# Kernel tuning notes

Hardware: AMD Instinct MI355X
Metric: run time of the kernel (lower is better)

Reference implementation:

```python
import jax, jax.numpy as jnp
import numpy as np

B, S, D, H = 2, 2048, 1024, 16
DH = D // H  # 64


def setup_inputs() -> dict:
    key = jax.random.key(0)
    ks = jax.random.split(key, 12)
    inp = {
        "hidden_states": jax.random.normal(ks[0], (B, S, D), dtype=jnp.float32),
        "attention_mask": jax.random.randint(ks[1], (B, S), 0, 2, dtype=jnp.int32),
        "Wq": jax.random.normal(ks[2], (D, D), dtype=jnp.float32) / np.sqrt(D),
        "bq": jnp.zeros((D,), dtype=jnp.float32),
        "Wk": jax.random.normal(ks[3], (D, D), dtype=jnp.float32) / np.sqrt(D),
        "bk": jnp.zeros((D,), dtype=jnp.float32),
        "Wv": jax.random.normal(ks[4], (D, D), dtype=jnp.float32) / np.sqrt(D),
        "bv": jnp.zeros((D,), dtype=jnp.float32),
        # per-head additive query bias (emotion manipulation path)
        "emotion_w": jax.random.normal(ks[5], (H, DH), dtype=jnp.float32),
        "Wo": jax.random.normal(ks[6], (D, D), dtype=jnp.float32) / np.sqrt(D),
        "bo": jnp.zeros((D,), dtype=jnp.float32),
    }
    return inp


def reference(hidden_states, attention_mask, Wq, bq, Wk, bk, Wv, bv, emotion_w, Wo, bo):
    b, s, d = hidden_states.shape
    # projections -> [b, h, s, dh]
    def proj(W, bias):
        y = hidden_states @ W + bias
        return y.reshape(b, s, H, DH).transpose(0, 2, 1, 3)

    q = proj(Wq, bq)
    k = proj(Wk, bk)
    v = proj(Wv, bv)

    # manipulation_type='emotion': additive per-head query bias
    q = q + emotion_w[None, :, None, :]

    scores = jnp.einsum("bhqd,bhkd->bhqk", q, k) / np.sqrt(DH).astype(np.float32)
    # key-padding mask: positions where mask==0 get -inf
    scores = jnp.where(attention_mask[:, None, None, :] == 0, -jnp.inf, scores)
    attn = jax.nn.softmax(scores, axis=-1)  # dropout is identity in eval mode

    out = jnp.einsum("bhqk,bhkd->bhqd", attn, v)
    out = out.transpose(0, 2, 1, 3).reshape(b, s, d)
    return out @ Wo + bo
```

## Files before the change

### kernel.cpp

```cpp
#include <hip/hip_runtime.h>
#include <hip/hip_bf16.h>


#define B_  2
#define S_  2048
#define D_  1024
#define K_  1024
#define H_  16
#define DH_ 64
#define BS_ (B_*S_)

typedef __hip_bfloat16 bf16;
typedef __attribute__((ext_vector_type(8))) short s8v;
typedef __attribute__((ext_vector_type(4))) short s4v;
typedef __attribute__((ext_vector_type(4))) float f4v;

__device__ __forceinline__ float b2f(bf16 x) { return __bfloat162float(x); }
__device__ __forceinline__ bf16  f2b(float x) { return __float2bfloat16(x); }

__device__ __forceinline__ void gl_lds_16B(const bf16* g, bf16* l) {
    __builtin_amdgcn_global_load_lds(
        (const __attribute__((address_space(1))) unsigned int*)g,
        (__attribute__((address_space(3))) unsigned int*)l, 16, 0, 0);
}

#define QSCALE_ 0.1803368801f

__global__ __launch_bounds__(256) void prep_kernel(
    const float* __restrict__ X, const int* __restrict__ mask,
    const float* __restrict__ Wq, const float* __restrict__ Wk,
    const float* __restrict__ Wv, const float* __restrict__ Wo,
    bf16* __restrict__ Xb, bf16* __restrict__ mkbf,
    bf16* __restrict__ WTq, bf16* __restrict__ WTk,
    bf16* __restrict__ WTv, bf16* __restrict__ WTo)
{
    __shared__ float Ls[64][68];
    const int blk = blockIdx.x;
    const int t   = threadIdx.x;

    if (blk < 1024) {
        const int z   = blk >> 8;
        const int t16 = blk & 255;
        const int k0  = (t16 >> 4) * 64;
        const int n0  = (t16 & 15) * 64;
        const float* __restrict__ W = (z == 0) ? Wq : (z == 1) ? Wk : (z == 2) ? Wv : Wo;
        bf16* __restrict__ WT       = (z == 0) ? WTq : (z == 1) ? WTk : (z == 2) ? WTv : WTo;

        const int lr = t >> 4;
        const int lc = (t & 15) * 4;
        #pragma unroll
        for (int i = 0; i < 4; i++) {
            const int k = i * 16 + lr;
            const float4 v = *(const float4*)(W + (size_t)(k0 + k) * K_ + n0 + lc);
            Ls[k][lc + 0] = v.x; Ls[k][lc + 1] = v.y;
            Ls[k][lc + 2] = v.z; Ls[k][lc + 3] = v.w;
        }
        __syncthreads();
        #pragma unroll
        for (int i = 0; i < 4; i++) {
            const int n = i * 16 + lr;
            s4v o;
            #pragma unroll
            for (int j = 0; j < 4; j++) {
                bf16 tb = f2b(Ls[lc + j][n]);
                o[j] = *(short*)&tb;
            }
            *(s4v*)(WT + (size_t)(n0 + n) * K_ + k0 + lc) = o;
        }
    } else if (blk < 5120) {
        const size_t idx = ((size_t)(blk - 1024) * 256 + t) * 4;
        const float4 v = *(const float4*)(X + idx);
        bf16 t0 = f2b(v.x), t1 = f2b(v.y), t2 = f2b(v.z), t3 = f2b(v.w);
        s4v o;
        o[0] = *(short*)&t0; o[1] = *(short*)&t1;
        o[2] = *(short*)&t2; o[3] = *(short*)&t3;
        *(s4v*)(Xb + idx) = o;
    } else {
        const int idx = (blk - 5120) * 256 + t;
        mkbf[idx] = f2b(mask[idx] ? 1.0f : 0.0f);
    }
}

template <bool SWAPPED>
__device__ __forceinline__ void gemm_tile(
    const bf16* __restrict__ A, const bf16* __restrict__ BT,
    int m0, int n0, bf16* As, bf16* Bs, f4v acc[4][4])
{
    const int t    = threadIdx.x;
    const int lane = t & 63;
    const int wave = t >> 6;
    const int quad = lane >> 4;
    const int l15  = lane & 15;
    const int wr   = wave >> 1;
    const int wc   = wave & 1;

    const int sr = t >> 3;
    const int sc = (t & 7) * 8;

    for (int kb = 0; kb < K_; kb += 64) {
        #pragma unroll
        for (int i = 0; i < 4; i++) {
            const int r = i * 32 + sr;
            gl_lds_16B(A  + (size_t)(m0 + r) * K_ + kb + sc, As + r * 64 + sc);
            gl_lds_16B(BT + (size_t)(n0 + r) * K_ + kb + sc, Bs + r * 64 + sc);
        }
        __syncthreads();

        #pragma unroll
        for (int ks = 0; ks < 2; ks++) {
            s8v fA[4], fB[4];
            #pragma unroll
            for (int i = 0; i < 4; i++) {
                fA[i] = *(const s8v*)&As[(wr * 64 + i * 16 + l15) * 64 + ks * 32 + quad * 8];
                fB[i] = *(const s8v*)&Bs[(wc * 64 + i * 16 + l15) * 64 + ks * 32 + quad * 8];
            }
            #pragma unroll
            for (int i = 0; i < 4; i++)
                #pragma unroll
                for (int j = 0; j < 4; j++)
                    acc[i][j] = SWAPPED
                        ? __builtin_amdgcn_mfma_f32_16x16x32_bf16(fB[i], fA[j], acc[i][j], 0, 0, 0)
                        : __builtin_amdgcn_mfma_f32_16x16x32_bf16(fA[i], fB[j], acc[i][j], 0, 0, 0);
        }
        __syncthreads();
    }
}

__global__ __launch_bounds__(256) void proj_qkv_kernel(
    const bf16* __restrict__ Xb,
    const bf16* __restrict__ WTq, const float* __restrict__ bq,
    const bf16* __restrict__ WTk, const float* __restrict__ bk,
    const bf16* __restrict__ WTv, const float* __restrict__ bv,
    const float* __restrict__ emo, const int* __restrict__ mask,
    bf16* __restrict__ q_ws, bf16* __restrict__ k_ws, bf16* __restrict__ v_ws)
{
    const int m0 = blockIdx.x * 128;
    const int n0 = blockIdx.y * 128;
    const int z  = blockIdx.z;

    __shared__ __align__(16) bf16 As[128 * 64];
    __shared__ __align__(16) bf16 Bs[128 * 64];

    const int t    = threadIdx.x;
    const int lane = t & 63;
    const int wave = t >> 6;
    const int quad = lane >> 4;
    const int l15  = lane & 15;
    const int wr   = wave >> 1;
    const int wc   = wave & 1;

    f4v acc[4][4] = {};

    if (z == 0) {
        gemm_tile<false>(Xb, WTq, m0, n0, As, Bs, acc);
        #pragma unroll
        for (int j = 0; j < 4; j++) {
            const int n  = n0 + wc * 64 + j * 16 + l15;
            const int h  = n >> 6, dh = n & 63;
            const float bias_n = bq[n] + emo[n];
            #pragma unroll
            for (int i = 0; i < 4; i++) {
                #pragma unroll
                for (int r = 0; r < 4; r++) {
                    const int m = m0 + wr * 64 + i * 16 + quad * 4 + r;
                    const int b = m >> 11, s = m & 2047;
                    q_ws[(((size_t)(b * H_ + h)) * S_ + s) * DH_ + dh] =
                        f2b((acc[i][j][r] + bias_n) * QSCALE_);
                }
            }
        }
    } else if (z == 1) {
        gemm_tile<false>(Xb, WTk, m0, n0, As, Bs, acc);
        #pragma unroll
        for (int j = 0; j < 4; j++) {
            const int n  = n0 + wc * 64 + j * 16 + l15;
            const int h  = n >> 6, dh = n & 63;
            const float bias_n = bk[n];
            #pragma unroll
            for (int i = 0; i < 4; i++) {
                #pragma unroll
                for (int r = 0; r < 4; r++) {
                    const int m = m0 + wr * 64 + i * 16 + quad * 4 + r;
                    const int b = m >> 11, s = m & 2047;
                    k_ws[(((size_t)(b * H_ + h)) * S_ + s) * DH_ + dh] =
                        f2b(acc[i][j][r] + bias_n);
                }
            }
        }
    } else {
        gemm_tile<true>(Xb, WTv, m0, n0, As, Bs, acc);
        #pragma unroll
        for (int j = 0; j < 4; j++) {
            const int m = m0 + wr * 64 + j * 16 + l15;
            const int b = m >> 11, s = m & 2047;
            const float msk = mask[b * S_ + s] ? 1.0f : 0.0f;
            #pragma unroll
            for (int i = 0; i < 4; i++) {
                #pragma unroll
                for (int r = 0; r < 4; r++) {
                    const int n  = n0 + wc * 64 + i * 16 + quad * 4 + r;
                    const int h  = n >> 6, dh = n & 63;
                    v_ws[(((size_t)(b * H_ + h)) * DH_ + dh) * S_ + s] =
                        f2b((acc[i][j][r] + bv[n]) * msk);
                }
            }
        }
    }
}

__global__ __launch_bounds__(256) void proj_out_kernel(
    const bf16* __restrict__ ctx, const bf16* __restrict__ WTo,
    const float* __restrict__ bo, float* __restrict__ out)
{
    const int m0 = blockIdx.x * 128;
    const int n0 = blockIdx.y * 128;

    __shared__ __align__(16) bf16 As[128 * 64];
    __shared__ __align__(16) bf16 Bs[128 * 64];

    const int t    = threadIdx.x;
    const int lane = t & 63;
    const int wave = t >> 6;
    const int quad = lane >> 4;
    const int l15  = lane & 15;
    const int wr   = wave >> 1;
    const int wc   = wave & 1;

    f4v acc[4][4] = {};
    gemm_tile<false>(ctx, WTo, m0, n0, As, Bs, acc);

    #pragma unroll
    for (int j = 0; j < 4; j++) {
        const int n = n0 + wc * 64 + j * 16 + l15;
        const float bias_n = bo[n];
        #pragma unroll
        for (int i = 0; i < 4; i++) {
            #pragma unroll
            for (int r = 0; r < 4; r++) {
                const int m = m0 + wr * 64 + i * 16 + quad * 4 + r;
                out[(size_t)m * D_ + n] = acc[i][j][r] + bias_n;
            }
        }
    }
}

#define PP_ 88

__global__ __launch_bounds__(512) void attn_kernel(
    const bf16* __restrict__ q_ws, const bf16* __restrict__ k_ws,
    const bf16* __restrict__ v_ws, const bf16* __restrict__ mkbf,
    bf16* __restrict__ ctx)
{
    const int bh = blockIdx.x;
    const int q0 = blockIdx.y * 128;
    const int b  = bh >> 4;
    const int h  = bh & 15;

    __shared__ __align__(16) bf16 k_lds[2][64 * 64];
    __shared__ __align__(16) bf16 vt_lds[2][64 * 64];
    __shared__ __align__(16) bf16 p_lds[8][16 * PP_];

    const int t    = threadIdx.x;
    const int wave = t >> 6;
    const int lane = t & 63;
    const int quad = lane >> 4;
    const int l15  = lane & 15;
    const int lxor = l15 & 7;

    s8v qf[2];
    #pragma unroll
    for (int dt = 0; dt < 2; dt++)
        qf[dt] = *(const s8v*)(q_ws +
            ((size_t)bh * S_ + q0 + wave * 16 + l15) * DH_ + dt * 32 + quad * 8);

    f4v oacc[4] = {};
    f4v osum   = {};

    const int r_st  = t >> 3;
    const int cs_st = (t & 7) ^ (r_st & 7);
    const int e_st  = t * 8;

    auto stage = [&](int kb0, bf16* kd, bf16* vd) {
        gl_lds_16B(k_ws + ((size_t)bh * S_ + kb0 + r_st) * DH_ + cs_st * 8,
                   kd + e_st);
        gl_lds_16B(v_ws + ((size_t)bh * DH_ + r_st) * S_ + kb0 + cs_st * 8,
                   vd + e_st);
    };

    stage(0, k_lds[0], vt_lds[0]);
    __syncthreads();

    int cur = 0;
    for (int kb0 = 0; kb0 < S_; kb0 += 64) {
        if (kb0 + 64 < S_)
            stage(kb0 + 64, k_lds[cur ^ 1], vt_lds[cur ^ 1]);

        const bf16* __restrict__ kc = k_lds[cur];
        const bf16* __restrict__ vc = vt_lds[cur];

        f4v sacc[4] = {};
        __builtin_amdgcn_s_setprio(1);
        #pragma unroll
        for (int kt = 0; kt < 4; kt++) {
            #pragma unroll
            for (int dt = 0; dt < 2; dt++) {
                const s8v kf = *(const s8v*)&kc[(kt * 16 + l15) * 64 +
                                                ((dt * 4 + quad) ^ lxor) * 8];
                sacc[kt] = __builtin_amdgcn_mfma_f32_16x16x32_bf16(kf, qf[dt], sacc[kt], 0, 0, 0);
            }
        }
        __builtin_amdgcn_s_setprio(0);

        #pragma unroll
        for (int kt = 0; kt < 4; kt++) {
            float2 e01, e23;
            e01.x = exp2f(sacc[kt][0]);
            e01.y = exp2f(sacc[kt][1]);
            e23.x = exp2f(sacc[kt][2]);
            e23.y = exp2f(sacc[kt][3]);
            union { __hip_bfloat162 hh; unsigned u; } lo, hi;
            lo.hh = __float22bfloat162_rn(e01);
            hi.hh = __float22bfloat162_rn(e23);
            *(uint2*)&p_lds[wave][l15 * PP_ + kt * 16 + quad * 4] =
                make_uint2(lo.u, hi.u);
        }

        __builtin_amdgcn_s_waitcnt(0xC07F);

        #pragma unroll
        for (int kh = 0; kh < 2; kh++) {
            const s8v ap = *(const s8v*)&p_lds[wave][l15 * PP_ + kh * 32 + quad * 8];
            const s8v mv = *(const s8v*)(mkbf + (size_t)b * S_ + kb0 + kh * 32 + quad * 8);
            __builtin_amdgcn_s_setprio(1);
            #pragma unroll
            for (int nt = 0; nt < 4; nt++) {
                const s8v vf = *(const s8v*)&vc[(nt * 16 + l15) * 64 +
                                                ((kh * 4 + quad) ^ lxor) * 8];
                oacc[nt] = __builtin_amdgcn_mfma_f32_16x16x32_bf16(ap, vf, oacc[nt], 0, 0, 0);
            }
            osum = __builtin_amdgcn_mfma_f32_16x16x32_bf16(ap, mv, osum, 0, 0, 0);
            __builtin_amdgcn_s_setprio(0);
        }

        __syncthreads();
        cur ^= 1;
    }

    #pragma unroll
    for (int r = 0; r < 4; r++) {
        const float inv = 1.0f / osum[r];
        const int q = q0 + wave * 16 + quad * 4 + r;
        #pragma unroll
        for (int nt = 0; nt < 4; nt++)
            ctx[((size_t)b * S_ + q) * D_ + h * DH_ + nt * 16 + l15] =
                f2b(oacc[nt][r] * inv);
    }
}

extern "C" void kernel_launch(void* const* d_in, const int* in_sizes, int n_in,
                              void* d_out, int out_size, void* d_ws, size_t ws_size,
                              hipStream_t stream) {
    (void)in_sizes; (void)n_in; (void)out_size; (void)ws_size;

    const float* X    = (const float*)d_in[0];
    const int*   mask = (const int*)d_in[1];
    const float* Wq   = (const float*)d_in[2];
    const float* bq   = (const float*)d_in[3];
    const float* Wk   = (const float*)d_in[4];
    const float* bk   = (const float*)d_in[5];
    const float* Wv   = (const float*)d_in[6];
    const float* bv   = (const float*)d_in[7];
    const float* emo  = (const float*)d_in[8];
    const float* Wo   = (const float*)d_in[9];
    const float* bo   = (const float*)d_in[10];
    float* out = (float*)d_out;

    bf16* q_ws = (bf16*)d_ws;
    bf16* k_ws = q_ws + (size_t)BS_ * D_;
    bf16* v_ws = k_ws + (size_t)BS_ * D_;
    bf16* ctx  = v_ws + (size_t)BS_ * D_;
    bf16* Xb   = ctx  + (size_t)BS_ * D_;
    bf16* WTq  = Xb   + (size_t)BS_ * D_;
    bf16* WTk  = WTq  + (size_t)D_ * K_;
    bf16* WTv  = WTk  + (size_t)D_ * K_;
    bf16* WTo  = WTv  + (size_t)D_ * K_;
    bf16* mkbf = WTo  + (size_t)D_ * K_;

    hipLaunchKernelGGL(prep_kernel, dim3(5136), dim3(256), 0, stream,
                       X, mask, Wq, Wk, Wv, Wo, Xb, mkbf, WTq, WTk, WTv, WTo);
    hipLaunchKernelGGL(proj_qkv_kernel, dim3(BS_ / 128, D_ / 128, 3), dim3(256), 0, stream,
                       Xb, WTq, bq, WTk, bk, WTv, bv, emo, mask, q_ws, k_ws, v_ws);
    hipLaunchKernelGGL(attn_kernel, dim3(B_ * H_, S_ / 128), dim3(512), 0, stream,
                       q_ws, k_ws, v_ws, mkbf, ctx);
    hipLaunchKernelGGL(proj_out_kernel, dim3(BS_ / 128, D_ / 128), dim3(256), 0, stream,
                       ctx, WTo, bo, out);
}
```

Before: 226.5 us.

## Rewrite attention with 32x32 MFMA tiles and direct global K/V fragment loads

The attention kernel moves from 16x16x32 MFMA tiles and 8 waves of 16 queries to 32x32x16 MFMA tiles and 4 waves of 32 queries each. K and V fragments are read straight from global memory (cache) instead of being staged into double-buffered LDS, which removes the per-block __syncthreads. The P tile is double-buffered by loop parity with an XOR swizzle. This trades away LDS staging and block-wide K/V sharing for fewer barriers and larger MFMA tiles, at the cost of more global/L2 traffic and fewer waves per block.

```diff
diff --git a/kernel.cpp b/kernel.cpp
--- a/kernel.cpp
+++ b/kernel.cpp
@@ -14,6 +14,7 @@
 typedef __attribute__((ext_vector_type(8))) short s8v;
 typedef __attribute__((ext_vector_type(4))) short s4v;
 typedef __attribute__((ext_vector_type(4))) float f4v;
+typedef __attribute__((ext_vector_type(16))) float f16v;
 
 __device__ __forceinline__ float b2f(bf16 x) { return __bfloat162float(x); }
 __device__ __forceinline__ bf16  f2b(float x) { return __float2bfloat16(x); }
@@ -244,9 +245,9 @@
     }
 }
 
-#define PP_ 88
-
-__global__ __launch_bounds__(512) void attn_kernel(
+#define PQ_ 2048
+
+__global__ __launch_bounds__(256) void attn_kernel(
     const bf16* __restrict__ q_ws, const bf16* __restrict__ k_ws,
     const bf16* __restrict__ v_ws, const bf16* __restrict__ mkbf,
     bf16* __restrict__ ctx)
@@ -256,104 +257,86 @@
     const int b  = bh >> 4;
     const int h  = bh & 15;
 
-    __shared__ __align__(16) bf16 k_lds[2][64 * 64];
-    __shared__ __align__(16) bf16 vt_lds[2][64 * 64];
-    __shared__ __align__(16) bf16 p_lds[8][16 * PP_];
+    __shared__ __align__(16) bf16 p_lds[2 * 4 * PQ_];
 
     const int t    = threadIdx.x;
     const int wave = t >> 6;
     const int lane = t & 63;
-    const int quad = lane >> 4;
-    const int l15  = lane & 15;
-    const int lxor = l15 & 7;
-
-    s8v qf[2];
+    const int ql   = lane & 31;
+    const int hf   = lane >> 5;
+    const int swz  = ql & 7;
+
+    s8v qf[4];
     #pragma unroll
-    for (int dt = 0; dt < 2; dt++)
-        qf[dt] = *(const s8v*)(q_ws +
-            ((size_t)bh * S_ + q0 + wave * 16 + l15) * DH_ + dt * 32 + quad * 8);
-
-    f4v oacc[4] = {};
-    f4v osum   = {};
-
-    const int r_st  = t >> 3;
-    const int cs_st = (t & 7) ^ (r_st & 7);
-    const int e_st  = t * 8;
-
-    auto stage = [&](int kb0, bf16* kd, bf16* vd) {
-        gl_lds_16B(k_ws + ((size_t)bh * S_ + kb0 + r_st) * DH_ + cs_st * 8,
-                   kd + e_st);
-        gl_lds_16B(v_ws + ((size_t)bh * DH_ + r_st) * S_ + kb0 + cs_st * 8,
-                   vd + e_st);
-    };
-
-    stage(0, k_lds[0], vt_lds[0]);
-    __syncthreads();
-
-    int cur = 0;
-    for (int kb0 = 0; kb0 < S_; kb0 += 64) {
-        if (kb0 + 64 < S_)
-            stage(kb0 + 64, k_lds[cur ^ 1], vt_lds[cur ^ 1]);
-
-        const bf16* __restrict__ kc = k_lds[cur];
-        const bf16* __restrict__ vc = vt_lds[cur];
-
-        f4v sacc[4] = {};
+    for (int kd = 0; kd < 4; kd++)
+        qf[kd] = *(const s8v*)(q_ws +
+            ((size_t)bh * S_ + q0 + wave * 32 + ql) * DH_ + kd * 16 + hf * 8);
+
+    f16v oacc[2] = {};
+    f16v osum    = {};
+
+    const bf16* __restrict__ kbase = k_ws + (size_t)bh * S_ * DH_;
+    const bf16* __restrict__ vbase = v_ws + (size_t)bh * DH_ * S_;
+    const bf16* __restrict__ mbase = mkbf + (size_t)b * S_;
+
+    int parity = 0;
+    for (int kb0 = 0; kb0 < S_; kb0 += 64, parity ^= 1) {
+        bf16* __restrict__ pb = p_lds + parity * (4 * PQ_) + wave * PQ_;
+
+        f16v sacc[2] = {};
         __builtin_amdgcn_s_setprio(1);
         #pragma unroll
-        for (int kt = 0; kt < 4; kt++) {
+        for (int kt = 0; kt < 2; kt++) {
+            #pragma unroll
+            for (int kd = 0; kd < 4; kd++) {
+                const s8v kf = *(const s8v*)(kbase +
+                    (size_t)(kb0 + kt * 32 + ql) * DH_ + kd * 16 + hf * 8);
+                sacc[kt] = __builtin_amdgcn_mfma_f32_32x32x16_bf16(kf, qf[kd], sacc[kt], 0, 0, 0);
+            }
+        }
+        __builtin_amdgcn_s_setprio(0);
+
+        #pragma unroll
+        for (int kt = 0; kt < 2; kt++) {
+            #pragma unroll
+            for (int g = 0; g < 4; g++) {
+                float2 e01, e23;
+                e01.x = exp2f(sacc[kt][4 * g + 0]);
+                e01.y = exp2f(sacc[kt][4 * g + 1]);
+                e23.x = exp2f(sacc[kt][4 * g + 2]);
+                e23.y = exp2f(sacc[kt][4 * g + 3]);
+                union { __hip_bfloat162 hh; unsigned u; } lo, hi;
+                lo.hh = __float22bfloat162_rn(e01);
+                hi.hh = __float22bfloat162_rn(e23);
+                *(uint2*)&pb[ql * 64 + ((kt * 4 + g) ^ swz) * 8 + hf * 4] =
+                    make_uint2(lo.u, hi.u);
+            }
+        }
+
+        #pragma unroll
+        for (int ks = 0; ks < 4; ks++) {
+            const s8v pf = *(const s8v*)&pb[ql * 64 + ((2 * ks + hf) ^ swz) * 8];
+            const s8v mf = *(const s8v*)(mbase + kb0 + ks * 16 + hf * 8);
+            __builtin_amdgcn_s_setprio(1);
+            osum = __builtin_amdgcn_mfma_f32_32x32x16_bf16(pf, mf, osum, 0, 0, 0);
             #pragma unroll
             for (int dt = 0; dt < 2; dt++) {
-                const s8v kf = *(const s8v*)&kc[(kt * 16 + l15) * 64 +
-                                                ((dt * 4 + quad) ^ lxor) * 8];
-                sacc[kt] = __builtin_amdgcn_mfma_f32_16x16x32_bf16(kf, qf[dt], sacc[kt], 0, 0, 0);
-            }
-        }
-        __builtin_amdgcn_s_setprio(0);
-
-        #pragma unroll
-        for (int kt = 0; kt < 4; kt++) {
-            float2 e01, e23;
-            e01.x = exp2f(sacc[kt][0]);
-            e01.y = exp2f(sacc[kt][1]);
-            e23.x = exp2f(sacc[kt][2]);
-            e23.y = exp2f(sacc[kt][3]);
-            union { __hip_bfloat162 hh; unsigned u; } lo, hi;
-            lo.hh = __float22bfloat162_rn(e01);
-            hi.hh = __float22bfloat162_rn(e23);
-            *(uint2*)&p_lds[wave][l15 * PP_ + kt * 16 + quad * 4] =
-                make_uint2(lo.u, hi.u);
-        }
-
-        __builtin_amdgcn_s_waitcnt(0xC07F);
-
-        #pragma unroll
-        for (int kh = 0; kh < 2; kh++) {
-            const s8v ap = *(const s8v*)&p_lds[wave][l15 * PP_ + kh * 32 + quad * 8];
-            const s8v mv = *(const s8v*)(mkbf + (size_t)b * S_ + kb0 + kh * 32 + quad * 8);
-            __builtin_amdgcn_s_setprio(1);
-            #pragma unroll
-            for (int nt = 0; nt < 4; nt++) {
-                const s8v vf = *(const s8v*)&vc[(nt * 16 + l15) * 64 +
-                                                ((kh * 4 + quad) ^ lxor) * 8];
-                oacc[nt] = __builtin_amdgcn_mfma_f32_16x16x32_bf16(ap, vf, oacc[nt], 0, 0, 0);
-            }
-            osum = __builtin_amdgcn_mfma_f32_16x16x32_bf16(ap, mv, osum, 0, 0, 0);
+                const s8v vf = *(const s8v*)(vbase +
+                    (size_t)(dt * 32 + ql) * S_ + kb0 + ks * 16 + hf * 8);
+                oacc[dt] = __builtin_amdgcn_mfma_f32_32x32x16_bf16(pf, vf, oacc[dt], 0, 0, 0);
+            }
             __builtin_amdgcn_s_setprio(0);
         }
-
-        __syncthreads();
-        cur ^= 1;
     }
 
     #pragma unroll
-    for (int r = 0; r < 4; r++) {
+    for (int r = 0; r < 16; r++) {
         const float inv = 1.0f / osum[r];
-        const int q = q0 + wave * 16 + quad * 4 + r;
-        #pragma unroll
-        for (int nt = 0; nt < 4; nt++)
-            ctx[((size_t)b * S_ + q) * D_ + h * DH_ + nt * 16 + l15] =
-                f2b(oacc[nt][r] * inv);
+        const int q = q0 + wave * 32 + (r & 3) + 8 * (r >> 2) + 4 * hf;
+        #pragma unroll
+        for (int dt = 0; dt < 2; dt++)
+            ctx[((size_t)b * S_ + q) * D_ + h * DH_ + dt * 32 + ql] =
+                f2b(oacc[dt][r] * inv);
     }
 }
 
@@ -390,7 +373,7 @@
                        X, mask, Wq, Wk, Wv, Wo, Xb, mkbf, WTq, WTk, WTv, WTo);
     hipLaunchKernelGGL(proj_qkv_kernel, dim3(BS_ / 128, D_ / 128, 3), dim3(256), 0, stream,
                        Xb, WTq, bq, WTk, bk, WTv, bv, emo, mask, q_ws, k_ws, v_ws);
-    hipLaunchKernelGGL(attn_kernel, dim3(B_ * H_, S_ / 128), dim3(512), 0, stream,
+    hipLaunchKernelGGL(attn_kernel, dim3(B_ * H_, S_ / 128), dim3(256), 0, stream,
                        q_ws, k_ws, v_ws, mkbf, ctx);
     hipLaunchKernelGGL(proj_out_kernel, dim3(BS_ / 128, D_ / 128), dim3(256), 0, stream,
                        ctx, WTo, bo, out);
```

Measured after the change: 293.6 us. 29.6% more time.
